# Kernel tuning notes

Measured on AMD Instinct MI355X. Metric: run time of the kernel, lower is better.

Reference implementation:

```python
import jax, jax.numpy as jnp
import numpy as np

B, S, E = 512, 200, 128
H, D = 4, 32  # att_head_nums, singlehead_emb_size; H*D == E (required by residual)
FF = 4 * H * D


def setup_inputs() -> dict:
    key = jax.random.key(0)
    ks = jax.random.split(key, 12)
    sc = 0.02
    return {
        "queries": jax.random.normal(ks[0], (B, S, E), jnp.float32),
        "keys": jax.random.normal(ks[1], (B, S, E), jnp.float32),
        "keys_mask": jax.random.randint(ks[2], (B, S), 0, 2) > 0,
        "Wq": jax.random.normal(ks[3], (H * D, E), jnp.float32) * sc,
        "bq": jnp.zeros((H * D,), jnp.float32),
        "Wk": jax.random.normal(ks[4], (H * D, E), jnp.float32) * sc,
        "bk": jnp.zeros((H * D,), jnp.float32),
        "Wv": jax.random.normal(ks[5], (H * D, E), jnp.float32) * sc,
        "bv": jnp.zeros((H * D,), jnp.float32),
        "W1": jax.random.normal(ks[6], (FF, H * D), jnp.float32) * sc,
        "b1": jnp.zeros((FF,), jnp.float32),
        "W2": jax.random.normal(ks[7], (H * D, FF), jnp.float32) * sc,
        "b2": jnp.zeros((H * D,), jnp.float32),
    }


def reference(queries, keys, keys_mask, Wq, bq, Wk, bk, Wv, bv, W1, b1, W2, b2):
    # QKV projections (nn.Linear: x @ W.T + b)
    Q = queries @ Wq.T + bq                         # [B,S,H*D]
    K = keys @ Wk.T + bk
    V = keys @ Wv.T + bv
    Qh = Q.reshape(B, S, H, D).transpose(0, 2, 1, 3)  # [B,H,S,D]
    Kh = K.reshape(B, S, H, D).transpose(0, 2, 1, 3)
    Vh = V.reshape(B, S, H, D).transpose(0, 2, 1, 3)
    scores = jnp.einsum('bhqd,bhkd->bhqk', Qh, Kh) / jnp.sqrt(jnp.float32(D))
    scores = jnp.where(keys_mask[:, None, None, :], scores, -jnp.inf)
    probs = jax.nn.softmax(scores, axis=-1)
    out = jnp.einsum('bhqk,bhkd->bhqd', probs, Vh)   # [B,H,S,D]
    out = out.transpose(0, 2, 1, 3).reshape(B, S, H * D)
    out = out + queries                              # residual (use_res=True)
    # FFN with residual (use_feed_forward=True, no layer norm, dropout=0)
    ff = jax.nn.relu(out @ W1.T + b1) @ W2.T + b2
    return ff + out
```

## Files before the change

### kernel.cpp

```cpp
#include <hip/hip_runtime.h>

#define B_  512
#define S_  200
#define M_  102400

typedef short bf16x8 __attribute__((ext_vector_type(8)));
typedef float f32x4  __attribute__((ext_vector_type(4)));
typedef unsigned short u16;
typedef u16 us4 __attribute__((ext_vector_type(4)));
typedef unsigned int u32;

#define MFMA16 __builtin_amdgcn_mfma_f32_16x16x32_bf16
#define GLDS(gp, lp) __builtin_amdgcn_global_load_lds( \
    (const __attribute__((address_space(1))) unsigned int*)(gp), \
    (__attribute__((address_space(3))) unsigned int*)(lp), 16, 0, 0)

__device__ __forceinline__ u16 f2bf(float f) {
    union { float f; unsigned u; } v; v.f = f;
    unsigned r = v.u + 0x7fffu + ((v.u >> 16) & 1u);
    return (u16)(r >> 16);
}
__device__ __forceinline__ float bf2f(u16 x) {
    union { unsigned u; float f; } v; v.u = ((unsigned)x) << 16;
    return v.f;
}
__device__ __forceinline__ u32 pk(float a, float b) {
    return (__float_as_uint(a) >> 16) | (__float_as_uint(b) & 0xffff0000u);
}
__device__ __forceinline__ int swz(int row, int b) { return b ^ ((row & 7) << 4); }

#define WQ_OFF   0
#define WK_OFF   16384
#define WV_OFF   32768
#define W1_OFF   49152
#define W2_OFF   114688
#define BQS_OFF  180224
#define QB_OFF   262144
#define KB_OFF   (QB_OFF + 13107200)
#define VB_OFF   (KB_OFF + 13107200)

__global__ __launch_bounds__(256) void cvt_kernel(
    const float* __restrict__ Wq, const float* __restrict__ bq,
    const float* __restrict__ Wk, const float* __restrict__ Wv,
    const float* __restrict__ W1, const float* __restrict__ W2,
    u16* __restrict__ wdst, float* __restrict__ bqs)
{
    const float QSC = 0.17677669529663689f * 1.4426950408889634f;
    int idx = blockIdx.x * 256 + threadIdx.x;
    if (idx < 128) bqs[idx] = bq[idx] * QSC;
    if (idx < 49152) {
        int wsel = idx >> 14, r = (idx >> 7) & 127, c = idx & 127;
        const float* src = wsel == 0 ? Wq : (wsel == 1 ? Wk : Wv);
        float v = src[idx & 16383];
        if (wsel == 0) v *= QSC;
        *(u16*)((char*)(wdst + wsel * 16384) + r * 256 + swz(r, 2 * c)) = f2bf(v);
    } else if (idx < 114688) {
        int i = idx - 49152;
        int r_g = i >> 7, c = i & 127;
        int sub = r_g >> 6, fr = r_g & 63;
        *(u16*)((char*)(wdst + W1_OFF) + sub * 16384 + fr * 256 + ((2 * c) ^ ((fr & 7) << 4)))
            = f2bf(W1[i]);
    } else if (idx < 180224) {
        int i = idx - 114688;
        int r_out = i >> 9, c_ff = i & 511;
        int sub = c_ff >> 6, o = c_ff & 63;
        int chunk = o >> 5, w32 = o & 31;
        int bb = w32 >> 4, hh = (w32 >> 2) & 3, rr = w32 & 3;
        int lc = chunk * 32 + 8 * hh + 4 * bb + rr;
        *(u16*)((char*)(wdst + W2_OFF) + sub * 16384 + r_out * 128 + ((2 * lc) ^ ((r_out & 7) << 4)))
            = f2bf(W2[i]);
    }
}

__global__ __launch_bounds__(256) void proj_q_kernel(
    const float* __restrict__ X, const u16* __restrict__ Ws,
    const float* __restrict__ bqs, u16* __restrict__ Y)
{
    __shared__ __align__(16) u16 sW[16384];
    const int tid = threadIdx.x, w = tid >> 6, lane = tid & 63;
    const int lo = lane & 15, hi = lane >> 4;
    const int base = blockIdx.x * 128;

#pragma unroll
    for (int k = 0; k < 8; ++k) {
        int seg = w * 8 + k;
        GLDS((const char*)Ws + seg * 1024 + lane * 16, (char*)sW + seg * 1024);
    }

    bf16x8 a[2][4];
#pragma unroll
    for (int t = 0; t < 2; ++t) {
        const float* rp = X + (size_t)(base + w * 32 + t * 16 + lo) * 128;
#pragma unroll
        for (int ks = 0; ks < 4; ++ks) {
            float4 v0 = *(const float4*)(rp + ks * 32 + hi * 8);
            float4 v1 = *(const float4*)(rp + ks * 32 + hi * 8 + 4);
            union { bf16x8 v; u16 s[8]; } af;
            af.s[0]=f2bf(v0.x); af.s[1]=f2bf(v0.y); af.s[2]=f2bf(v0.z); af.s[3]=f2bf(v0.w);
            af.s[4]=f2bf(v1.x); af.s[5]=f2bf(v1.y); af.s[6]=f2bf(v1.z); af.s[7]=f2bf(v1.w);
            a[t][ks] = af.v;
        }
    }
    asm volatile("s_waitcnt vmcnt(0)" ::: "memory");
    __builtin_amdgcn_s_barrier();

#pragma unroll
    for (int n = 0; n < 8; ++n) {
        bf16x8 bf[4];
#pragma unroll
        for (int ks = 0; ks < 4; ++ks)
            bf[ks] = *(const bf16x8*)((const char*)sW + (n*16+lo)*256 + swz(lo, ks*64 + hi*16));
        float bb = bqs[n * 16 + lo];
#pragma unroll
        for (int t = 0; t < 2; ++t) {
            f32x4 acc = {0.f, 0.f, 0.f, 0.f};
#pragma unroll
            for (int ks = 0; ks < 4; ++ks) acc = MFMA16(a[t][ks], bf[ks], acc, 0, 0, 0);
#pragma unroll
            for (int r = 0; r < 4; ++r) {
                int row = base + w * 32 + t * 16 + hi * 4 + r;
                *(u16*)((char*)Y + (size_t)row * 256 + swz(row, n * 32 + 2 * lo)) =
                    f2bf(acc[r] + bb);
            }
        }
    }
}

__global__ __launch_bounds__(256) void proj_kv_kernel(
    const float* __restrict__ X, const u16* __restrict__ Wks, const u16* __restrict__ Wvs,
    const float* __restrict__ bk, const float* __restrict__ bv,
    u16* __restrict__ K, u16* __restrict__ V)
{
    __shared__ __align__(16) u16 sWk[16384];
    __shared__ __align__(16) u16 sWv[16384];
    const int tid = threadIdx.x, w = tid >> 6, lane = tid & 63;
    const int lo = lane & 15, hi = lane >> 4;
    const int base = blockIdx.x * 128;

#pragma unroll
    for (int k = 0; k < 8; ++k) {
        int seg = w * 8 + k;
        GLDS((const char*)Wks + seg * 1024 + lane * 16, (char*)sWk + seg * 1024);
        GLDS((const char*)Wvs + seg * 1024 + lane * 16, (char*)sWv + seg * 1024);
    }

    bf16x8 a[2][4];
#pragma unroll
    for (int t = 0; t < 2; ++t) {
        const float* rp = X + (size_t)(base + w * 32 + t * 16 + lo) * 128;
#pragma unroll
        for (int ks = 0; ks < 4; ++ks) {
            float4 v0 = *(const float4*)(rp + ks * 32 + hi * 8);
            float4 v1 = *(const float4*)(rp + ks * 32 + hi * 8 + 4);
            union { bf16x8 v; u16 s[8]; } af;
            af.s[0]=f2bf(v0.x); af.s[1]=f2bf(v0.y); af.s[2]=f2bf(v0.z); af.s[3]=f2bf(v0.w);
            af.s[4]=f2bf(v1.x); af.s[5]=f2bf(v1.y); af.s[6]=f2bf(v1.z); af.s[7]=f2bf(v1.w);
            a[t][ks] = af.v;
        }
    }
    asm volatile("s_waitcnt vmcnt(0)" ::: "memory");
    __builtin_amdgcn_s_barrier();

#pragma unroll
    for (int n = 0; n < 8; ++n) {
        bf16x8 bf[4];
#pragma unroll
        for (int ks = 0; ks < 4; ++ks)
            bf[ks] = *(const bf16x8*)((const char*)sWk + (n*16+lo)*256 + swz(lo, ks*64 + hi*16));
        float bb = bk[n * 16 + lo];
#pragma unroll
        for (int t = 0; t < 2; ++t) {
            f32x4 acc = {0.f, 0.f, 0.f, 0.f};
#pragma unroll
            for (int ks = 0; ks < 4; ++ks) acc = MFMA16(a[t][ks], bf[ks], acc, 0, 0, 0);
#pragma unroll
            for (int r = 0; r < 4; ++r) {
                size_t row = base + w * 32 + t * 16 + hi * 4 + r;
                K[row * 128 + n * 16 + lo] = f2bf(acc[r] + bb);
            }
        }
    }
#pragma unroll
    for (int n = 0; n < 8; ++n) {
        bf16x8 bf[4];
#pragma unroll
        for (int ks = 0; ks < 4; ++ks)
            bf[ks] = *(const bf16x8*)((const char*)sWv + (n*16+lo)*256 + swz(lo, ks*64 + hi*16));
        float bb = bv[n * 16 + lo];
#pragma unroll
        for (int t = 0; t < 2; ++t) {
            f32x4 acc = {0.f, 0.f, 0.f, 0.f};
#pragma unroll
            for (int ks = 0; ks < 4; ++ks) acc = MFMA16(a[t][ks], bf[ks], acc, 0, 0, 0);
#pragma unroll
            for (int r = 0; r < 4; ++r) {
                size_t row = base + w * 32 + t * 16 + hi * 4 + r;
                V[row * 128 + n * 16 + lo] = f2bf(acc[r] + bb);
            }
        }
    }
}

__global__ __launch_bounds__(256, 4) void attn_kernel(
    const u16* __restrict__ Qb, const u16* __restrict__ Kb, const u16* __restrict__ Vb,
    const int* __restrict__ mask, const float* __restrict__ queries, u16* __restrict__ Xb)
{
    __shared__ __align__(16) u16 sK[224][40];
    __shared__ __align__(16) u16 sVt[32][248];
    __shared__ __align__(16) u16 sMk[224];
    __shared__ u16 sIdx[224];
    __shared__ int sCnt4[4];

    const int bid = blockIdx.x;
    const int wg  = (bid & 7) * 256 + (bid >> 3);
    const int b   = wg >> 2;
    const int h   = wg & 3;
    const int tid = threadIdx.x;
    const int w = tid >> 6, lane = tid & 63;
    const int lo = lane & 15, hi = lane >> 4;
    const size_t rowbase = (size_t)b * 200;

    bool valid = (tid < 200) && (mask[rowbase + tid] != 0);
    unsigned long long bal = __ballot(valid);
    int prefix = __popcll(bal & ((1ull << lane) - 1ull));
    if (lane == 0) sCnt4[w] = __popcll(bal);
    __syncthreads();

    int c0_ = sCnt4[0], c1_ = sCnt4[1], c2_ = sCnt4[2], c3_ = sCnt4[3];
    int off = (w > 0 ? c0_ : 0) + (w > 1 ? c1_ : 0) + (w > 2 ? c2_ : 0);
    const int cnt = c0_ + c1_ + c2_ + c3_;
    const int cntPad = (cnt + 31) & ~31;
    const int nch = cntPad >> 5;
    if (valid) sIdx[off + prefix] = (u16)tid;
    for (int i = tid; i < 224; i += 256) {
        int cb = i & ~31, local = i & 31;
        int hh = local >> 3, j = local & 7;
        int slot = cb + 16 * (j >> 2) + 4 * hh + (j & 3);
        sMk[i] = (slot < cnt) ? (u16)0x3F80 : (u16)0;
    }
    __syncthreads();

    for (int i = tid; i < (cntPad << 2); i += 256) {
        int j = i >> 2, part = i & 3;
        bf16x8 val = {0,0,0,0,0,0,0,0};
        if (j < cnt) {
            int key = sIdx[j];
            val = *(const bf16x8*)(Kb + (rowbase + key) * 128 + h * 32 + part * 8);
        }
        *(bf16x8*)&sK[j][part * 8] = val;
    }
    for (int slot = tid; slot < (cntPad << 3); slot += 256) {
        int d = slot & 31, sg = slot >> 5;
        int s0 = sg * 4;
        int cb = s0 & ~31, a = (s0 & 31) >> 2;
        int pos = cb + (a & 3) * 8 + (a >> 2) * 4;
        us4 v;
#pragma unroll
        for (int j = 0; j < 4; ++j) {
            int s = s0 + j;
            v[j] = (s < cnt) ? Vb[(rowbase + sIdx[s]) * 128 + h * 32 + d] : (u16)0;
        }
        *(us4*)&sVt[d][pos] = v;
    }
    __syncthreads();

    for (int qb = w; qb < 13; qb += 4) {
        int qrow = qb * 16 + lo;
        if (qrow > 199) qrow = 199;
        bf16x8 qf = *(const bf16x8*)((const char*)Qb + (size_t)(rowbase + qrow) * 256
                                      + swz(qrow, h * 64 + hi * 16));

        f32x4 acc0 = {0.f, 0.f, 0.f, 0.f};
        f32x4 acc1 = {0.f, 0.f, 0.f, 0.f};
        f32x4 accs = {0.f, 0.f, 0.f, 0.f};

#pragma unroll 1
        for (int kt = 0; kt < nch; ++kt) {
            int cb = kt * 32;
            bf16x8 k0 = *(const bf16x8*)&sK[cb + lo][hi * 8];
            bf16x8 k1 = *(const bf16x8*)&sK[cb + 16 + lo][hi * 8];
            f32x4 z = {0.f, 0.f, 0.f, 0.f};
            f32x4 s0 = MFMA16(k0, qf, z, 0, 0, 0);
            f32x4 s1 = MFMA16(k1, qf, z, 0, 0, 0);
            float p0 = __builtin_amdgcn_exp2f(s0[0]);
            float p1 = __builtin_amdgcn_exp2f(s0[1]);
            float p2 = __builtin_amdgcn_exp2f(s0[2]);
            float p3 = __builtin_amdgcn_exp2f(s0[3]);
            float p4 = __builtin_amdgcn_exp2f(s1[0]);
            float p5 = __builtin_amdgcn_exp2f(s1[1]);
            float p6 = __builtin_amdgcn_exp2f(s1[2]);
            float p7 = __builtin_amdgcn_exp2f(s1[3]);
            union { bf16x8 v; u32 d[4]; } pa;
            pa.d[0] = pk(p0, p1); pa.d[1] = pk(p2, p3);
            pa.d[2] = pk(p4, p5); pa.d[3] = pk(p6, p7);
            bf16x8 mkf = *(const bf16x8*)&sMk[cb + hi * 8];
            bf16x8 v0  = *(const bf16x8*)&sVt[lo][cb + hi * 8];
            bf16x8 v1  = *(const bf16x8*)&sVt[16 + lo][cb + hi * 8];
            acc0 = MFMA16(pa.v, v0, acc0, 0, 0, 0);
            acc1 = MFMA16(pa.v, v1, acc1, 0, 0, 0);
            accs = MFMA16(pa.v, mkf, accs, 0, 0, 0);
        }

        float invr[4];
#pragma unroll
        for (int r = 0; r < 4; ++r) invr[r] = __builtin_amdgcn_rcpf(accs[r]);
#pragma unroll
        for (int r = 0; r < 4; ++r) {
            int row = qb * 16 + hi * 4 + r;
            if (row < 200) {
                size_t o  = (rowbase + row) * 128 + h * 32;
                size_t rb = (rowbase + row) * 256;
                *(u16*)((char*)Xb + rb + swz(row, h * 64 + 2 * lo)) =
                    f2bf(acc0[r] * invr[r] + queries[o + lo]);
                *(u16*)((char*)Xb + rb + swz(row, h * 64 + 32 + 2 * lo)) =
                    f2bf(acc1[r] * invr[r] + queries[o + 16 + lo]);
            }
        }
    }
}

__global__ __launch_bounds__(256, 2) void ffn_kernel(
    const u16* __restrict__ Xb, const u16* __restrict__ W1s, const u16* __restrict__ W2s,
    const float* __restrict__ b1, const float* __restrict__ b2, float* __restrict__ out)
{
    __shared__ __align__(16) u16 sW1[2][8192];
    __shared__ __align__(16) u16 sW2[2][8192];
    const int tid = threadIdx.x, w = tid >> 6, lane = tid & 63;
    const int lo = lane & 15, hi = lane >> 4;
    const size_t base = (size_t)blockIdx.x * 128;
    const int wrow = w * 32;

#pragma unroll
    for (int k = 0; k < 4; ++k) {
        int seg = w * 4 + k;
        GLDS((const char*)W1s + seg * 1024 + lane * 16, (char*)sW1[0] + seg * 1024);
        GLDS((const char*)W2s + seg * 1024 + lane * 16, (char*)sW2[0] + seg * 1024);
    }

    bf16x8 a[2][4];
#pragma unroll
    for (int t = 0; t < 2; ++t) {
        size_t row = base + wrow + t * 16 + lo;
#pragma unroll
        for (int ks = 0; ks < 4; ++ks)
            a[t][ks] = *(const bf16x8*)((const char*)Xb + row * 256
                                         + ((ks * 64 + hi * 16) ^ ((lo & 7) << 4)));
    }

    f32x4 yacc[2][8];
#pragma unroll
    for (int t = 0; t < 2; ++t)
#pragma unroll
        for (int n = 0; n < 8; ++n) yacc[t][n] = (f32x4){0.f, 0.f, 0.f, 0.f};

    asm volatile("s_waitcnt vmcnt(0)" ::: "memory");
    __builtin_amdgcn_s_barrier();

    for (int sub = 0; sub < 8; ++sub) {
        int cur = sub & 1, nxt = cur ^ 1;
        if (sub < 7) {
#pragma unroll
            for (int k = 0; k < 4; ++k) {
                int seg = w * 4 + k;
                GLDS((const char*)W1s + (sub + 1) * 16384 + seg * 1024 + lane * 16,
                     (char*)sW1[nxt] + seg * 1024);
                GLDS((const char*)W2s + (sub + 1) * 16384 + seg * 1024 + lane * 16,
                     (char*)sW2[nxt] + seg * 1024);
            }
        }
#pragma unroll
        for (int c = 0; c < 2; ++c) {
            bf16x8 w1f[2][4];
#pragma unroll
            for (int u = 0; u < 2; ++u)
#pragma unroll
                for (int ks = 0; ks < 4; ++ks)
                    w1f[u][ks] = *(const bf16x8*)((const char*)sW1[cur]
                                   + ((2*c+u) * 16 + lo) * 256
                                   + ((ks * 64 + hi * 16) ^ ((lo & 7) << 4)));
            float4 b1v0 = *(const float4*)(b1 + sub * 64 + (2*c) * 16 + 4 * hi);
            float4 b1v1 = *(const float4*)(b1 + sub * 64 + (2*c+1) * 16 + 4 * hi);
            bf16x8 pb[2];
#pragma unroll
            for (int t = 0; t < 2; ++t) {
                f32x4 h0 = {0.f,0.f,0.f,0.f}, h1 = {0.f,0.f,0.f,0.f};
#pragma unroll
                for (int ks = 0; ks < 4; ++ks) {
                    h0 = MFMA16(w1f[0][ks], a[t][ks], h0, 0, 0, 0);
                    h1 = MFMA16(w1f[1][ks], a[t][ks], h1, 0, 0, 0);
                }
                float p0 = fmaxf(h0[0] + b1v0.x, 0.f);
                float p1 = fmaxf(h0[1] + b1v0.y, 0.f);
                float p2 = fmaxf(h0[2] + b1v0.z, 0.f);
                float p3 = fmaxf(h0[3] + b1v0.w, 0.f);
                float p4 = fmaxf(h1[0] + b1v1.x, 0.f);
                float p5 = fmaxf(h1[1] + b1v1.y, 0.f);
                float p6 = fmaxf(h1[2] + b1v1.z, 0.f);
                float p7 = fmaxf(h1[3] + b1v1.w, 0.f);
                union { bf16x8 v; u32 d[4]; } pu;
                pu.d[0] = pk(p0, p1); pu.d[1] = pk(p2, p3);
                pu.d[2] = pk(p4, p5); pu.d[3] = pk(p6, p7);
                pb[t] = pu.v;
            }
#pragma unroll
            for (int n = 0; n < 8; ++n) {
                bf16x8 w2f = *(const bf16x8*)((const char*)sW2[cur]
                               + (n * 16 + lo) * 128
                               + ((c * 64 + hi * 16) ^ ((lo & 7) << 4)));
                yacc[0][n] = MFMA16(w2f, pb[0], yacc[0][n], 0, 0, 0);
                yacc[1][n] = MFMA16(w2f, pb[1], yacc[1][n], 0, 0, 0);
            }
        }
        asm volatile("s_waitcnt vmcnt(0)" ::: "memory");
        __builtin_amdgcn_s_barrier();
    }

#pragma unroll
    for (int t = 0; t < 2; ++t) {
        size_t row = base + wrow + t * 16 + lo;
#pragma unroll
        for (int n = 0; n < 8; ++n) {
            float4 b2v = *(const float4*)(b2 + n * 16 + 4 * hi);
            us4 rv = *(const us4*)((const char*)Xb + row * 256
                                    + ((2 * (n * 16 + 4 * hi)) ^ (((int)row & 7) << 4)));
            float4 o;
            o.x = yacc[t][n][0] + b2v.x + bf2f(rv[0]);
            o.y = yacc[t][n][1] + b2v.y + bf2f(rv[1]);
            o.z = yacc[t][n][2] + b2v.z + bf2f(rv[2]);
            o.w = yacc[t][n][3] + b2v.w + bf2f(rv[3]);
            *(float4*)(out + row * 128 + n * 16 + 4 * hi) = o;
        }
    }
}

extern "C" void kernel_launch(void* const* d_in, const int* in_sizes, int n_in,
                              void* d_out, int out_size, void* d_ws, size_t ws_size,
                              hipStream_t stream) {
    const float* queries = (const float*)d_in[0];
    const float* keys    = (const float*)d_in[1];
    const int*   mask    = (const int*)d_in[2];
    const float* Wq = (const float*)d_in[3];
    const float* bq = (const float*)d_in[4];
    const float* Wk = (const float*)d_in[5];
    const float* bk = (const float*)d_in[6];
    const float* Wv = (const float*)d_in[7];
    const float* bv = (const float*)d_in[8];
    const float* W1 = (const float*)d_in[9];
    const float* b1 = (const float*)d_in[10];
    const float* W2 = (const float*)d_in[11];
    const float* b2 = (const float*)d_in[12];
    float* out = (float*)d_out;

    u16* wbase = (u16*)d_ws;
    u16* Qb = wbase + QB_OFF;
    u16* Kb = wbase + KB_OFF;
    u16* Vb = wbase + VB_OFF;
    float* bqs = (float*)(wbase + BQS_OFF);

    cvt_kernel<<<704, 256, 0, stream>>>(Wq, bq, Wk, Wv, W1, W2, wbase, bqs);
    proj_q_kernel<<<800, 256, 0, stream>>>(queries, wbase + WQ_OFF, bqs, Qb);
    proj_kv_kernel<<<800, 256, 0, stream>>>(keys, wbase + WK_OFF, wbase + WV_OFF,
                                            bk, bv, Kb, Vb);
    attn_kernel<<<B_ * 4, 256, 0, stream>>>(Qb, Kb, Vb, mask, queries, Qb);
    ffn_kernel<<<800, 256, 0, stream>>>(Qb, wbase + W1_OFF, wbase + W2_OFF, b1, b2, out);
}
```

Before: 127.9 us.

## Read FFN weights directly from global memory instead of LDS double-buffering

The FFN kernel stops staging W1/W2 into double-buffered shared memory with barriers. Each wave now loads weight fragments straight from global memory (L2/L1-cached), in 32-column sub-chunks with a repacked W2 layout produced by the conversion kernel. This removes the LDS traffic, barriers and the 64KB of LDS per block, which may raise occupancy. In exchange it relies on cache hits for weight reuse across waves and exposes global-load latency inside the MFMA loop.

```diff
diff --git a/kernel.cpp b/kernel.cpp
--- a/kernel.cpp
+++ b/kernel.cpp
@@ -57,18 +57,17 @@
     } else if (idx < 114688) {
         int i = idx - 49152;
         int r_g = i >> 7, c = i & 127;
-        int sub = r_g >> 6, fr = r_g & 63;
-        *(u16*)((char*)(wdst + W1_OFF) + sub * 16384 + fr * 256 + ((2 * c) ^ ((fr & 7) << 4)))
+        int sub = r_g >> 5, fr = r_g & 31;
+        *(u16*)((char*)(wdst + W1_OFF) + sub * 8192 + fr * 256 + ((2 * c) ^ ((fr & 7) << 4)))
             = f2bf(W1[i]);
     } else if (idx < 180224) {
         int i = idx - 114688;
         int r_out = i >> 9, c_ff = i & 511;
-        int sub = c_ff >> 6, o = c_ff & 63;
-        int chunk = o >> 5, w32 = o & 31;
+        int s32 = c_ff >> 5, w32 = c_ff & 31;
         int bb = w32 >> 4, hh = (w32 >> 2) & 3, rr = w32 & 3;
-        int lc = chunk * 32 + 8 * hh + 4 * bb + rr;
-        *(u16*)((char*)(wdst + W2_OFF) + sub * 16384 + r_out * 128 + ((2 * lc) ^ ((r_out & 7) << 4)))
-            = f2bf(W2[i]);
+        int lc = 8 * hh + 4 * bb + rr;
+        *(u16*)((char*)(wdst + W2_OFF) + s32 * 8192 + r_out * 64
+                + ((2 * lc) ^ (((r_out >> 1) & 3) << 4))) = f2bf(W2[i]);
     }
 }
 
@@ -323,20 +322,11 @@
     const u16* __restrict__ Xb, const u16* __restrict__ W1s, const u16* __restrict__ W2s,
     const float* __restrict__ b1, const float* __restrict__ b2, float* __restrict__ out)
 {
-    __shared__ __align__(16) u16 sW1[2][8192];
-    __shared__ __align__(16) u16 sW2[2][8192];
     const int tid = threadIdx.x, w = tid >> 6, lane = tid & 63;
     const int lo = lane & 15, hi = lane >> 4;
     const size_t base = (size_t)blockIdx.x * 128;
     const int wrow = w * 32;
 
-#pragma unroll
-    for (int k = 0; k < 4; ++k) {
-        int seg = w * 4 + k;
-        GLDS((const char*)W1s + seg * 1024 + lane * 16, (char*)sW1[0] + seg * 1024);
-        GLDS((const char*)W2s + seg * 1024 + lane * 16, (char*)sW2[0] + seg * 1024);
-    }
-
     bf16x8 a[2][4];
 #pragma unroll
     for (int t = 0; t < 2; ++t) {
@@ -353,66 +343,51 @@
 #pragma unroll
         for (int n = 0; n < 8; ++n) yacc[t][n] = (f32x4){0.f, 0.f, 0.f, 0.f};
 
-    asm volatile("s_waitcnt vmcnt(0)" ::: "memory");
-    __builtin_amdgcn_s_barrier();
-
-    for (int sub = 0; sub < 8; ++sub) {
-        int cur = sub & 1, nxt = cur ^ 1;
-        if (sub < 7) {
-#pragma unroll
-            for (int k = 0; k < 4; ++k) {
-                int seg = w * 4 + k;
-                GLDS((const char*)W1s + (sub + 1) * 16384 + seg * 1024 + lane * 16,
-                     (char*)sW1[nxt] + seg * 1024);
-                GLDS((const char*)W2s + (sub + 1) * 16384 + seg * 1024 + lane * 16,
-                     (char*)sW2[nxt] + seg * 1024);
+    const int w1off0 = (0 * 16 + lo) * 256;
+    const int w1off1 = (1 * 16 + lo) * 256;
+    const int w2swz  = (hi * 16) ^ (((lo >> 1) & 3) << 4);
+
+#pragma unroll 4
+    for (int s = 0; s < 16; ++s) {
+        const char* w1p = (const char*)W1s + s * 8192;
+        const char* w2p = (const char*)W2s + s * 8192;
+        bf16x8 w1f[2][4];
+#pragma unroll
+        for (int ks = 0; ks < 4; ++ks) {
+            int co = (ks * 64 + hi * 16) ^ ((lo & 7) << 4);
+            w1f[0][ks] = *(const bf16x8*)(w1p + w1off0 + co);
+            w1f[1][ks] = *(const bf16x8*)(w1p + w1off1 + co);
+        }
+        float4 b1v0 = *(const float4*)(b1 + s * 32 + 4 * hi);
+        float4 b1v1 = *(const float4*)(b1 + s * 32 + 16 + 4 * hi);
+        bf16x8 pb[2];
+#pragma unroll
+        for (int t = 0; t < 2; ++t) {
+            f32x4 h0 = {0.f,0.f,0.f,0.f}, h1 = {0.f,0.f,0.f,0.f};
+#pragma unroll
+            for (int ks = 0; ks < 4; ++ks) {
+                h0 = MFMA16(w1f[0][ks], a[t][ks], h0, 0, 0, 0);
+                h1 = MFMA16(w1f[1][ks], a[t][ks], h1, 0, 0, 0);
             }
-        }
-#pragma unroll
-        for (int c = 0; c < 2; ++c) {
-            bf16x8 w1f[2][4];
-#pragma unroll
-            for (int u = 0; u < 2; ++u)
-#pragma unroll
-                for (int ks = 0; ks < 4; ++ks)
-                    w1f[u][ks] = *(const bf16x8*)((const char*)sW1[cur]
-                                   + ((2*c+u) * 16 + lo) * 256
-                                   + ((ks * 64 + hi * 16) ^ ((lo & 7) << 4)));
-            float4 b1v0 = *(const float4*)(b1 + sub * 64 + (2*c) * 16 + 4 * hi);
-            float4 b1v1 = *(const float4*)(b1 + sub * 64 + (2*c+1) * 16 + 4 * hi);
-            bf16x8 pb[2];
-#pragma unroll
-            for (int t = 0; t < 2; ++t) {
-                f32x4 h0 = {0.f,0.f,0.f,0.f}, h1 = {0.f,0.f,0.f,0.f};
-#pragma unroll
-                for (int ks = 0; ks < 4; ++ks) {
-                    h0 = MFMA16(w1f[0][ks], a[t][ks], h0, 0, 0, 0);
-                    h1 = MFMA16(w1f[1][ks], a[t][ks], h1, 0, 0, 0);
-                }
-                float p0 = fmaxf(h0[0] + b1v0.x, 0.f);
-                float p1 = fmaxf(h0[1] + b1v0.y, 0.f);
-                float p2 = fmaxf(h0[2] + b1v0.z, 0.f);
-                float p3 = fmaxf(h0[3] + b1v0.w, 0.f);
-                float p4 = fmaxf(h1[0] + b1v1.x, 0.f);
-                float p5 = fmaxf(h1[1] + b1v1.y, 0.f);
-                float p6 = fmaxf(h1[2] + b1v1.z, 0.f);
-                float p7 = fmaxf(h1[3] + b1v1.w, 0.f);
-                union { bf16x8 v; u32 d[4]; } pu;
-                pu.d[0] = pk(p0, p1); pu.d[1] = pk(p2, p3);
-                pu.d[2] = pk(p4, p5); pu.d[3] = pk(p6, p7);
-                pb[t] = pu.v;
-            }
-#pragma unroll
-            for (int n = 0; n < 8; ++n) {
-                bf16x8 w2f = *(const bf16x8*)((const char*)sW2[cur]
-                               + (n * 16 + lo) * 128
-                               + ((c * 64 + hi * 16) ^ ((lo & 7) << 4)));
-                yacc[0][n] = MFMA16(w2f, pb[0], yacc[0][n], 0, 0, 0);
-                yacc[1][n] = MFMA16(w2f, pb[1], yacc[1][n], 0, 0, 0);
-            }
-        }
-        asm volatile("s_waitcnt vmcnt(0)" ::: "memory");
-        __builtin_amdgcn_s_barrier();
+            float p0 = fmaxf(h0[0] + b1v0.x, 0.f);
+            float p1 = fmaxf(h0[1] + b1v0.y, 0.f);
+            float p2 = fmaxf(h0[2] + b1v0.z, 0.f);
+            float p3 = fmaxf(h0[3] + b1v0.w, 0.f);
+            float p4 = fmaxf(h1[0] + b1v1.x, 0.f);
+            float p5 = fmaxf(h1[1] + b1v1.y, 0.f);
+            float p6 = fmaxf(h1[2] + b1v1.z, 0.f);
+            float p7 = fmaxf(h1[3] + b1v1.w, 0.f);
+            union { bf16x8 v; u32 d[4]; } pu;
+            pu.d[0] = pk(p0, p1); pu.d[1] = pk(p2, p3);
+            pu.d[2] = pk(p4, p5); pu.d[3] = pk(p6, p7);
+            pb[t] = pu.v;
+        }
+#pragma unroll
+        for (int n = 0; n < 8; ++n) {
+            bf16x8 w2f = *(const bf16x8*)(w2p + (n * 16 + lo) * 64 + w2swz);
+            yacc[0][n] = MFMA16(w2f, pb[0], yacc[0][n], 0, 0, 0);
+            yacc[1][n] = MFMA16(w2f, pb[1], yacc[1][n], 0, 0, 0);
+        }
     }
 
 #pragma unroll
```

After: 180.0 us. 40.7% more time.
